# Kernel optimization log

Measured on AMD Instinct MI355X. Metric: run time of the kernel, lower is better.

Reference implementation:

```python
import jax, jax.numpy as jnp
import numpy as np

POPULATION = 1000000.0  # __init__ arg of MarkovChainRNN_Model
B, T, F = 16384, 2048, 2  # batch, timesteps, (beta, gamma) per step


def setup_inputs() -> dict:
    key = jax.random.key(0)
    k1, k2 = jax.random.split(key)
    # per-step (beta, gamma) rates in [0, 1)
    inputs = jax.random.uniform(k1, (B, T, F), dtype=jnp.float32)
    # initial [S, I, R] state; scaled so S+I+R is O(population)
    initial_state = jax.random.uniform(k2, (B, 3), dtype=jnp.float32) * POPULATION
    return {"inputs": inputs, "initial_state": initial_state}


def reference(inputs, initial_state):
    # SIR cell update, one step per day:
    #   new_inf = beta * S * I / N ; new_rec = gamma * I
    #   S' = S - new_inf ; I' = I + new_inf - new_rec ; R' = R + new_rec
    # Keras RNN(cell, return_state=True) -> (last_output, last_state);
    # for an SIR cell output == state, so both returns are the final state.
    def step(state, u):
        beta, gamma = u[:, 0], u[:, 1]            # [B], [B]
        S, I, R = state[:, 0], state[:, 1], state[:, 2]
        new_inf = beta * S * I / POPULATION
        new_rec = gamma * I
        new_state = jnp.stack([S - new_inf,
                               I + new_inf - new_rec,
                               R + new_rec], axis=-1)  # [B, 3]
        return new_state, None

    xs = jnp.transpose(inputs, (1, 0, 2))  # time-major [T, B, F]
    final_state, _ = jax.lax.scan(step, initial_state, xs)
    return (final_state, final_state)
```

## Files before the change

### kernel.cpp

```cpp
#include <hip/hip_runtime.h>
#include <stdint.h>
#include <stddef.h>


#define T_STEPS 2048
#define C_STEPS 64
#define NCHUNK  (T_STEPS / C_STEPS)
#define BPB     64
#define PAIRS   (C_STEPS / 2)
#define INSTR_PER_CHUNK 32

#define INV_POP 1e-6f

__device__ __forceinline__ void stage_chunk(const float* __restrict__ in,
                                            float4* lds, int b0, int c, int lane)
{
    const int hi = lane >> 5;
    const int q  = lane & 31;
#pragma unroll
    for (int j = 0; j < INSTR_PER_CHUNK; ++j) {
        const int bi = 2 * j + hi;
        const int p  = q ^ (bi & 15);
        const float* g = in
            + (size_t)(b0 + bi) * (T_STEPS * 2)
            + (size_t)c * (C_STEPS * 2)
            + (size_t)(p * 4);
        float4* l = lds + j * 64;
        __builtin_amdgcn_global_load_lds(
            (__attribute__((address_space(1))) void*)g,
            (__attribute__((address_space(3))) void*)l,
            16, 0, 0);
    }
}

__device__ __forceinline__ void compute_chunk(const float4* lds, int tid,
                                              float& S, float& I, float& R)
{
    const int swz = tid & 15;
    const float4* row = lds + tid * PAIRS;
#pragma unroll
    for (int p = 0; p < PAIRS; ++p) {
        const float4 v = row[p ^ swz];

        float ni = S * I * (v.x * INV_POP);
        float nr = v.y * I;
        S = S - ni;
        I = I + ni - nr;
        R = R + nr;

        ni = S * I * (v.z * INV_POP);
        nr = v.w * I;
        S = S - ni;
        I = I + ni - nr;
        R = R + nr;
    }
}

__global__ __launch_bounds__(64)
void sir_scan_kernel(const float* __restrict__ in, const float* __restrict__ init,
                     float* __restrict__ out, int half)
{
    __shared__ float4 bufA[BPB * PAIRS];
    __shared__ float4 bufB[BPB * PAIRS];

    const int tid = threadIdx.x;
    const int b0  = blockIdx.x * BPB;
    const int gb  = b0 + tid;

    float S = init[gb * 3 + 0];
    float I = init[gb * 3 + 1];
    float R = init[gb * 3 + 2];

    stage_chunk(in, bufA, b0, 0, tid);

#pragma unroll 1
    for (int c = 0; c < NCHUNK; c += 2) {
        asm volatile("s_waitcnt vmcnt(0)" ::: "memory");
        if (c + 1 < NCHUNK) stage_chunk(in, bufB, b0, c + 1, tid);
        compute_chunk(bufA, tid, S, I, R);

        asm volatile("s_waitcnt vmcnt(0)" ::: "memory");
        if (c + 2 < NCHUNK) stage_chunk(in, bufA, b0, c + 2, tid);
        compute_chunk(bufB, tid, S, I, R);
    }

    out[gb * 3 + 0] = S;
    out[gb * 3 + 1] = I;
    out[gb * 3 + 2] = R;
    out[half + gb * 3 + 0] = S;
    out[half + gb * 3 + 1] = I;
    out[half + gb * 3 + 2] = R;
}

extern "C" void kernel_launch(void* const* d_in, const int* in_sizes, int n_in,
                              void* d_out, int out_size, void* d_ws, size_t ws_size,
                              hipStream_t stream) {
    (void)in_sizes; (void)n_in; (void)d_ws; (void)ws_size;
    const float* in   = (const float*)d_in[0];
    const float* init = (const float*)d_in[1];
    float* out        = (float*)d_out;
    const int half = out_size / 2;

    dim3 grid(16384 / BPB);
    dim3 block(BPB);
    sir_scan_kernel<<<grid, block, 0, stream>>>(in, init, out, half);
}
```

Before: 61.83 us.

## Deepen LDS staging pipeline to four buffers with partial vmcnt waits

Halves the chunk size to 32 steps and rotates through four LDS buffers, keeping three chunks of global->LDS loads in flight. Partial s_waitcnt vmcnt(32/16) replaces full drains, so compute on one chunk overlaps with several outstanding loads. The aim is to hide more memory latency on this bandwidth-bound scan. LDS use per block stays the same, but correctness now depends on the exact count of in-flight load instructions and on there being no other vector memory ops in between.

```diff
diff --git a/kernel.cpp b/kernel.cpp
--- a/kernel.cpp
+++ b/kernel.cpp
@@ -4,22 +4,22 @@
 
 
 #define T_STEPS 2048
-#define C_STEPS 64
+#define C_STEPS 32
 #define NCHUNK  (T_STEPS / C_STEPS)
 #define BPB     64
 #define PAIRS   (C_STEPS / 2)
-#define INSTR_PER_CHUNK 32
+#define IPC     16
 
 #define INV_POP 1e-6f
 
 __device__ __forceinline__ void stage_chunk(const float* __restrict__ in,
                                             float4* lds, int b0, int c, int lane)
 {
-    const int hi = lane >> 5;
-    const int q  = lane & 31;
+    const int sub = lane >> 4;
+    const int q   = lane & 15;
 #pragma unroll
-    for (int j = 0; j < INSTR_PER_CHUNK; ++j) {
-        const int bi = 2 * j + hi;
+    for (int j = 0; j < IPC; ++j) {
+        const int bi = 4 * j + sub;
         const int p  = q ^ (bi & 15);
         const float* g = in
             + (size_t)(b0 + bi) * (T_STEPS * 2)
@@ -56,12 +56,18 @@
     }
 }
 
+#define WAIT32() asm volatile("s_waitcnt vmcnt(32)" ::: "memory")
+#define WAIT16() asm volatile("s_waitcnt vmcnt(16)" ::: "memory")
+#define WAIT0()  asm volatile("s_waitcnt vmcnt(0)"  ::: "memory")
+
 __global__ __launch_bounds__(64)
 void sir_scan_kernel(const float* __restrict__ in, const float* __restrict__ init,
                      float* __restrict__ out, int half)
 {
-    __shared__ float4 bufA[BPB * PAIRS];
-    __shared__ float4 bufB[BPB * PAIRS];
+    __shared__ float4 buf0[BPB * PAIRS];
+    __shared__ float4 buf1[BPB * PAIRS];
+    __shared__ float4 buf2[BPB * PAIRS];
+    __shared__ float4 buf3[BPB * PAIRS];
 
     const int tid = threadIdx.x;
     const int b0  = blockIdx.x * BPB;
@@ -71,18 +77,30 @@
     float I = init[gb * 3 + 1];
     float R = init[gb * 3 + 2];
 
-    stage_chunk(in, bufA, b0, 0, tid);
+    stage_chunk(in, buf0, b0, 0, tid);
+    stage_chunk(in, buf1, b0, 1, tid);
+    stage_chunk(in, buf2, b0, 2, tid);
 
 #pragma unroll 1
-    for (int c = 0; c < NCHUNK; c += 2) {
-        asm volatile("s_waitcnt vmcnt(0)" ::: "memory");
-        if (c + 1 < NCHUNK) stage_chunk(in, bufB, b0, c + 1, tid);
-        compute_chunk(bufA, tid, S, I, R);
+    for (int c = 0; c < NCHUNK - 4; c += 4) {
+        WAIT32(); stage_chunk(in, buf3, b0, c + 3, tid);
+        compute_chunk(buf0, tid, S, I, R);
+        WAIT32(); stage_chunk(in, buf0, b0, c + 4, tid);
+        compute_chunk(buf1, tid, S, I, R);
+        WAIT32(); stage_chunk(in, buf1, b0, c + 5, tid);
+        compute_chunk(buf2, tid, S, I, R);
+        WAIT32(); stage_chunk(in, buf2, b0, c + 6, tid);
+        compute_chunk(buf3, tid, S, I, R);
+    }
 
-        asm volatile("s_waitcnt vmcnt(0)" ::: "memory");
-        if (c + 2 < NCHUNK) stage_chunk(in, bufA, b0, c + 2, tid);
-        compute_chunk(bufB, tid, S, I, R);
-    }
+    WAIT32(); stage_chunk(in, buf3, b0, NCHUNK - 1, tid);
+    compute_chunk(buf0, tid, S, I, R);
+    WAIT32();
+    compute_chunk(buf1, tid, S, I, R);
+    WAIT16();
+    compute_chunk(buf2, tid, S, I, R);
+    WAIT0();
+    compute_chunk(buf3, tid, S, I, R);
 
     out[gb * 3 + 0] = S;
     out[gb * 3 + 1] = I;
```

New measurement: 81.48 us. 1.32x slower.

## Warp-specialize SIR scan into producer and consumer waves with 4-deep LDS ring

Applied to the files above, without the earlier changes.

Splits each block into a compute wave and a separate loader wave. The loader streams chunks into a four-buffer LDS ring with global_load_lds, keeping two chunks in flight, and the two waves hand off buffers through s_barrier. This takes load issue and vmcnt waits off the serial recurrence's critical path. In exchange LDS use doubles, each block has a second wave, and every chunk now needs a block barrier. The cross-wave visibility of async LDS writes relies on the loader's vmcnt wait happening before the barrier.

```diff
diff --git a/kernel.cpp b/kernel.cpp
--- a/kernel.cpp
+++ b/kernel.cpp
@@ -8,7 +8,7 @@
 #define NCHUNK  (T_STEPS / C_STEPS)
 #define BPB     64
 #define PAIRS   (C_STEPS / 2)
-#define INSTR_PER_CHUNK 32
+#define IPC     32
 
 #define INV_POP 1e-6f
 
@@ -18,7 +18,7 @@
     const int hi = lane >> 5;
     const int q  = lane & 31;
 #pragma unroll
-    for (int j = 0; j < INSTR_PER_CHUNK; ++j) {
+    for (int j = 0; j < IPC; ++j) {
         const int bi = 2 * j + hi;
         const int p  = q ^ (bi & 15);
         const float* g = in
@@ -56,40 +56,60 @@
     }
 }
 
-__global__ __launch_bounds__(64)
+#define BAR()   asm volatile("s_barrier" ::: "memory")
+#define WAIT32() asm volatile("s_waitcnt vmcnt(32)" ::: "memory")
+#define WAIT0()  asm volatile("s_waitcnt vmcnt(0)"  ::: "memory")
+
+__global__ __launch_bounds__(128)
 void sir_scan_kernel(const float* __restrict__ in, const float* __restrict__ init,
                      float* __restrict__ out, int half)
 {
-    __shared__ float4 bufA[BPB * PAIRS];
-    __shared__ float4 bufB[BPB * PAIRS];
+    __shared__ float4 buf0[BPB * PAIRS];
+    __shared__ float4 buf1[BPB * PAIRS];
+    __shared__ float4 buf2[BPB * PAIRS];
+    __shared__ float4 buf3[BPB * PAIRS];
 
     const int tid = threadIdx.x;
     const int b0  = blockIdx.x * BPB;
-    const int gb  = b0 + tid;
 
-    float S = init[gb * 3 + 0];
-    float I = init[gb * 3 + 1];
-    float R = init[gb * 3 + 2];
-
-    stage_chunk(in, bufA, b0, 0, tid);
+    if (tid < 64) {
+        const int gb = b0 + tid;
+        float S = init[gb * 3 + 0];
+        float I = init[gb * 3 + 1];
+        float R = init[gb * 3 + 2];
 
 #pragma unroll 1
-    for (int c = 0; c < NCHUNK; c += 2) {
-        asm volatile("s_waitcnt vmcnt(0)" ::: "memory");
-        if (c + 1 < NCHUNK) stage_chunk(in, bufB, b0, c + 1, tid);
-        compute_chunk(bufA, tid, S, I, R);
+        for (int c = 0; c < NCHUNK; c += 4) {
+            BAR(); compute_chunk(buf0, tid, S, I, R);
+            BAR(); compute_chunk(buf1, tid, S, I, R);
+            BAR(); compute_chunk(buf2, tid, S, I, R);
+            BAR(); compute_chunk(buf3, tid, S, I, R);
+        }
 
-        asm volatile("s_waitcnt vmcnt(0)" ::: "memory");
-        if (c + 2 < NCHUNK) stage_chunk(in, bufA, b0, c + 2, tid);
-        compute_chunk(bufB, tid, S, I, R);
+        out[gb * 3 + 0] = S;
+        out[gb * 3 + 1] = I;
+        out[gb * 3 + 2] = R;
+        out[half + gb * 3 + 0] = S;
+        out[half + gb * 3 + 1] = I;
+        out[half + gb * 3 + 2] = R;
+    } else {
+        const int lane = tid - 64;
+
+        stage_chunk(in, buf0, b0, 0, lane);
+        stage_chunk(in, buf1, b0, 1, lane);
+
+#pragma unroll 1
+        for (int c = 0; c < NCHUNK - 4; c += 4) {
+            WAIT32(); BAR(); stage_chunk(in, buf2, b0, c + 2, lane);
+            WAIT32(); BAR(); stage_chunk(in, buf3, b0, c + 3, lane);
+            WAIT32(); BAR(); stage_chunk(in, buf0, b0, c + 4, lane);
+            WAIT32(); BAR(); stage_chunk(in, buf1, b0, c + 5, lane);
+        }
+        WAIT32(); BAR(); stage_chunk(in, buf2, b0, NCHUNK - 2, lane);
+        WAIT32(); BAR(); stage_chunk(in, buf3, b0, NCHUNK - 1, lane);
+        WAIT32(); BAR();
+        WAIT0();  BAR();
     }
-
-    out[gb * 3 + 0] = S;
-    out[gb * 3 + 1] = I;
-    out[gb * 3 + 2] = R;
-    out[half + gb * 3 + 0] = S;
-    out[half + gb * 3 + 1] = I;
-    out[half + gb * 3 + 2] = R;
 }
 
 extern "C" void kernel_launch(void* const* d_in, const int* in_sizes, int n_in,
@@ -102,6 +122,6 @@
     const int half = out_size / 2;
 
     dim3 grid(16384 / BPB);
-    dim3 block(BPB);
+    dim3 block(128);
     sir_scan_kernel<<<grid, block, 0, stream>>>(in, init, out, half);
 }
```

Measured after the change: 57.45 us. 7.1% less time.

## Use 8 batch rows per block with redundant lanes and deeper prefetch pipeline

Applied to the files above, without the earlier changes.

Each 64-thread block now handles 8 batch rows instead of 64. Each row is computed redundantly by 8 lanes (tid&7), which gives 2048 blocks instead of 256 and spreads the work across far more CUs. Chunks grow to 128 steps, the XOR swizzle is adjusted to match, and two chunks are kept in flight using partial vmcnt waits instead of draining to zero. The cost is that 7/8 of the ALU lanes do duplicate work, and each block loads only 8 rows per chunk.

```diff
diff --git a/kernel.cpp b/kernel.cpp
--- a/kernel.cpp
+++ b/kernel.cpp
@@ -4,25 +4,22 @@
 
 
 #define T_STEPS 2048
-#define C_STEPS 64
+#define C_STEPS 128
 #define NCHUNK  (T_STEPS / C_STEPS)
-#define BPB     64
-#define PAIRS   (C_STEPS / 2)
-#define INSTR_PER_CHUNK 32
+#define BPB     8
+#define GRAN    (C_STEPS / 2)
+#define IPC     8
 
 #define INV_POP 1e-6f
 
 __device__ __forceinline__ void stage_chunk(const float* __restrict__ in,
                                             float4* lds, int b0, int c, int lane)
 {
-    const int hi = lane >> 5;
-    const int q  = lane & 31;
 #pragma unroll
-    for (int j = 0; j < INSTR_PER_CHUNK; ++j) {
-        const int bi = 2 * j + hi;
-        const int p  = q ^ (bi & 15);
+    for (int j = 0; j < IPC; ++j) {
+        const int p = lane ^ j;
         const float* g = in
-            + (size_t)(b0 + bi) * (T_STEPS * 2)
+            + (size_t)(b0 + j) * (T_STEPS * 2)
             + (size_t)c * (C_STEPS * 2)
             + (size_t)(p * 4);
         float4* l = lds + j * 64;
@@ -33,13 +30,13 @@
     }
 }
 
-__device__ __forceinline__ void compute_chunk(const float4* lds, int tid,
+__device__ __forceinline__ void compute_chunk(const float4* lds, int r,
                                               float& S, float& I, float& R)
 {
-    const int swz = tid & 15;
-    const float4* row = lds + tid * PAIRS;
+    const int swz = r & 7;
+    const float4* row = lds + r * GRAN;
 #pragma unroll
-    for (int p = 0; p < PAIRS; ++p) {
+    for (int p = 0; p < GRAN; ++p) {
         const float4 v = row[p ^ swz];
 
         float ni = S * I * (v.x * INV_POP);
@@ -56,40 +53,50 @@
     }
 }
 
+#define WAIT8() asm volatile("s_waitcnt vmcnt(8)" ::: "memory")
+#define WAIT0() asm volatile("s_waitcnt vmcnt(0)" ::: "memory")
+
 __global__ __launch_bounds__(64)
 void sir_scan_kernel(const float* __restrict__ in, const float* __restrict__ init,
                      float* __restrict__ out, int half)
 {
-    __shared__ float4 bufA[BPB * PAIRS];
-    __shared__ float4 bufB[BPB * PAIRS];
+    __shared__ float4 bufA[BPB * GRAN];
+    __shared__ float4 bufB[BPB * GRAN];
 
     const int tid = threadIdx.x;
     const int b0  = blockIdx.x * BPB;
-    const int gb  = b0 + tid;
+    const int r   = tid & 7;
+    const int gb  = b0 + r;
 
     float S = init[gb * 3 + 0];
     float I = init[gb * 3 + 1];
     float R = init[gb * 3 + 2];
 
     stage_chunk(in, bufA, b0, 0, tid);
+    stage_chunk(in, bufB, b0, 1, tid);
 
 #pragma unroll 1
-    for (int c = 0; c < NCHUNK; c += 2) {
-        asm volatile("s_waitcnt vmcnt(0)" ::: "memory");
-        if (c + 1 < NCHUNK) stage_chunk(in, bufB, b0, c + 1, tid);
-        compute_chunk(bufA, tid, S, I, R);
+    for (int c = 0; c < NCHUNK - 2; c += 2) {
+        WAIT8();
+        compute_chunk(bufA, r, S, I, R);
+        stage_chunk(in, bufA, b0, c + 2, tid);
+        WAIT8();
+        compute_chunk(bufB, r, S, I, R);
+        stage_chunk(in, bufB, b0, c + 3, tid);
+    }
+    WAIT8();
+    compute_chunk(bufA, r, S, I, R);
+    WAIT0();
+    compute_chunk(bufB, r, S, I, R);
 
-        asm volatile("s_waitcnt vmcnt(0)" ::: "memory");
-        if (c + 2 < NCHUNK) stage_chunk(in, bufA, b0, c + 2, tid);
-        compute_chunk(bufB, tid, S, I, R);
+    if (tid < 8) {
+        out[gb * 3 + 0] = S;
+        out[gb * 3 + 1] = I;
+        out[gb * 3 + 2] = R;
+        out[half + gb * 3 + 0] = S;
+        out[half + gb * 3 + 1] = I;
+        out[half + gb * 3 + 2] = R;
     }
-
-    out[gb * 3 + 0] = S;
-    out[gb * 3 + 1] = I;
-    out[gb * 3 + 2] = R;
-    out[half + gb * 3 + 0] = S;
-    out[half + gb * 3 + 1] = I;
-    out[half + gb * 3 + 2] = R;
 }
 
 extern "C" void kernel_launch(void* const* d_in, const int* in_sizes, int n_in,
@@ -102,6 +109,6 @@
     const int half = out_size / 2;
 
     dim3 grid(16384 / BPB);
-    dim3 block(BPB);
+    dim3 block(64);
     sir_scan_kernel<<<grid, block, 0, stream>>>(in, init, out, half);
 }
```

Result: slower. 201.6 us (+226.0%).
